# Kernel tuning notes

Measured on AMD Instinct MI355X. Metric: run time of the kernel, lower is better.

Reference implementation:

```python
import jax, jax.numpy as jnp
import numpy as np

B, L, D, V = 4096, 200, 64, 100000
ATTR_LEN = (2, 6, 10)  # label_size = 18
NEG = -1e9


def setup_inputs() -> dict:
    key = jax.random.key(0)
    ks = jax.random.split(key, 12)
    x = jax.random.randint(ks[0], (B, L), 0, V)
    lengths = jax.random.randint(ks[1], (B,), 1, L + 1)  # ragged valid lengths >= 1
    x_mask = jnp.arange(L)[None, :] < lengths[:, None]   # prefix-valid bool mask [B,L]
    y = (jax.random.uniform(ks[2], (B, sum(ATTR_LEN))) < 0.5).astype(jnp.float32)
    ob = (jax.random.uniform(ks[3], (B, sum(ATTR_LEN))) < 0.8).astype(jnp.float32)
    emb_table = (jax.random.normal(ks[4], (V, D)) * 0.02).at[0].set(0.0)  # padding_idx=0
    tran_W = jax.random.normal(ks[5], (3, D, D)) * 0.05   # emb_tran Linear weights (per attr)
    tran_b = jnp.zeros((3, D))
    att_W = jax.random.normal(ks[6], (3, D)) * 0.05       # item_att_W: Linear(D,1) per attr
    att_b = jnp.zeros((3,))
    W0 = jax.random.normal(ks[7], (D, ATTR_LEN[0])) * 0.05  # W_all (no bias)
    W1 = jax.random.normal(ks[8], (D, ATTR_LEN[1])) * 0.05
    W2 = jax.random.normal(ks[9], (D, ATTR_LEN[2])) * 0.05
    return {"x": x, "x_mask": x_mask, "y": y, "ob": ob, "emb_table": emb_table,
            "tran_W": tran_W, "tran_b": tran_b, "att_W": att_W, "att_b": att_b,
            "W0": W0, "W1": W1, "W2": W2}


def reference(x, x_mask, y, ob, emb_table, tran_W, tran_b, att_W, att_b, W0, W1, W2):
    # embed: [B,L,D]
    embed = emb_table[x]
    # per-attribute transformed embeddings: [3,B,L,D]
    e = jax.nn.relu(jnp.einsum('bld,ade->able', embed, tran_W) + tran_b[:, None, None, :])
    # attention logits per attribute: [3,B,L]
    att_u = jax.nn.relu(jnp.einsum('able,ae->abl', e, att_W) + att_b[:, None, None])
    # masked softmax over valid prefix (equivalent to the per-sample length loop)
    m = x_mask.astype(e.dtype)
    scores = jnp.where(x_mask[None, :, :], att_u, NEG)
    att = jax.nn.softmax(scores, axis=-1) * m[None, :, :]
    # attention-pooled user representation per attribute: [3,B,D]
    rep = jnp.tanh(jnp.einsum('abl,able->abe', att, e))
    # torch: cat([rep_a.unsqueeze(2)],2).view(B,-1) -> interleaved (d-major, attr-minor) layout
    user_flat = jnp.transpose(rep, (1, 2, 0)).reshape(rep.shape[1], -1)  # [B, 3*D]
    Ddim = emb_table.shape[1]
    W_user = jnp.concatenate([user_flat[:, 0 * Ddim:1 * Ddim] @ W0,
                              user_flat[:, 1 * Ddim:2 * Ddim] @ W1,
                              user_flat[:, 2 * Ddim:3 * Ddim] @ W2], axis=1)
    # W_compact = W_user * ob  (observed-label mask)
    return W_user * ob
```

## Files before the change

kernel.cpp:

```cpp
#include <hip/hip_runtime.h>

typedef unsigned int u32;
typedef unsigned short u16;
typedef unsigned char u8;
typedef unsigned long long u64;

typedef __attribute__((ext_vector_type(8))) short bf16x8;
typedef __attribute__((ext_vector_type(4))) float f32x4;
typedef __attribute__((ext_vector_type(4))) u32 u32x4;

#define L_SEQ 200

__device__ __forceinline__ u16 f2bf(float f) {
    u32 u = __float_as_uint(f);
    return (u16)((u + 0x7FFFu + ((u >> 16) & 1u)) >> 16);
}
__device__ __forceinline__ u32 pk2bf(float fx, float fy) {
    u32 xb = __float_as_uint(fx) + 0x8000u;
    u32 yb = __float_as_uint(fy) + 0x8000u;
    return __byte_perm(xb, yb, 0x7632);
}

__device__ __forceinline__ float row16_sum(float v) {
    int x;
    x = __builtin_amdgcn_update_dpp(0, __float_as_int(v), 0x128, 0xF, 0xF, true);
    v += __int_as_float(x);
    x = __builtin_amdgcn_update_dpp(0, __float_as_int(v), 0x124, 0xF, 0xF, true);
    v += __int_as_float(x);
    x = __builtin_amdgcn_update_dpp(0, __float_as_int(v), 0x122, 0xF, 0xF, true);
    v += __int_as_float(x);
    x = __builtin_amdgcn_update_dpp(0, __float_as_int(v), 0x121, 0xF, 0xF, true);
    v += __int_as_float(x);
    return v;
}
__device__ __forceinline__ float wave_sumf(float v) {
    v = row16_sum(v);
    v += __shfl_xor(v, 16, 64);
    v += __shfl_xor(v, 32, 64);
    return v;
}

__global__ __launch_bounds__(256) void etna_prep(const void* __restrict__ xmask,
                                                 const float* __restrict__ tranW,
                                                 const float* __restrict__ emb,
                                                 void* __restrict__ ws, int Bn, int Vn,
                                                 int doConv) {
    const int tid = threadIdx.x;
    const int bid = blockIdx.x;

    if (doConv) {
        u64* dst = (u64*)((char*)ws + 40960);
        const float4* src = (const float4*)emb;
        int ng = Vn * 16;
        for (int i = bid * 256 + tid; i < ng; i += gridDim.x * 256) {
            float4 v = src[i];
            u64 lo = pk2bf(v.x, v.y);
            u64 hi = pk2bf(v.z, v.w);
            dst[i] = lo | (hi << 32);
        }
    }

    if (bid < 48) {
        int it = bid * 256 + tid;
        int jj = it & 7;
        int ln = (it >> 3) & 63;
        int kh = (it >> 9) & 1;
        int c = (it >> 10) & 3;
        int a = it >> 12;
        int k = kh * 32 + (ln >> 4) * 8 + jj;
        int n = c * 16 + (ln & 15);
        ((u16*)ws)[it] = f2bf(tranW[a * 4096 + k * 64 + n]);
        return;
    }

    const int wv = tid >> 6;
    const int lane = tid & 63;
    int esz;
    {
        u32 accF = 0, acc0 = 0, accO = 0;
#pragma unroll
        for (int k = 0; k < 4; ++k) {
            int i = lane + 64 * k;
            u32 w = (i < 200) ? ((const u32*)xmask)[i] : 0u;
            accF |= (w & 0xFEFEFEFEu);
            acc0 |= (w & 0x000000FFu);
            accO |= (w & 0xFFFFFF00u);
        }
        bool isFloat = __ballot(accF != 0) != 0;
        bool hasB0   = __ballot(acc0 != 0) != 0;
        bool hasOdd  = __ballot(accO != 0) != 0;
        esz = isFloat ? (hasB0 ? 2 : 4) : (hasOdd ? 1 : 4);
    }
    int s = (bid - 48) * 4 + wv;
    if (s < Bn) {
        int len = 0;
        int mbase = s * L_SEQ;
#pragma unroll
        for (int c4 = 0; c4 < 4; ++c4) {
            int l = c4 * 64 + lane;
            bool v = false;
            if (l < L_SEQ) {
                int off = mbase + l;
                if (esz == 1)      v = ((const u8*)xmask)[off] != 0;
                else if (esz == 2) v = ((const u16*)xmask)[off] != 0;
                else               v = ((const u32*)xmask)[off] != 0;
            }
            len += (int)__popcll(__ballot(v));
        }
        if (lane == 0) ((int*)((char*)ws + 24576))[s] = len;
    }
}

template <bool TAB>
__global__ __launch_bounds__(384, 4) void etna_mfma(
    const int* __restrict__ x, const float* __restrict__ ob,
    const float* __restrict__ emb, const float* __restrict__ tranb,
    const float* __restrict__ attW, const float* __restrict__ attb,
    const float* __restrict__ W0, const float* __restrict__ W1,
    const float* __restrict__ W2, float* __restrict__ out,
    const void* __restrict__ ws, int Vn) {
    __shared__ float pN[2][3][64];
    __shared__ float pD[2][3];
    __shared__ float repl[3][64];

    const int tid = threadIdx.x;
    const int w = tid >> 6;
    const int a = w % 3;
    const int h = w / 3;
    const int lane = tid & 63;
    const int col = lane & 15;
    const int g = lane >> 4;
    const int b = blockIdx.x;

    const u16* wsBf = (const u16*)ws;
    bf16x8 Bf[4][2];
#pragma unroll
    for (int c = 0; c < 4; ++c)
#pragma unroll
        for (int kh = 0; kh < 2; ++kh)
            Bf[c][kh] = *(const bf16x8*)&wsBf[(((a * 4 + c) * 2 + kh) * 64 + lane) * 8];

    const int len = ((const int*)((const char*)ws + 24576))[b];
    const u16* wsEmb = (const u16*)((const char*)ws + 40960);

    const float LOG2E = 1.44269504088896f;
    float TB[4], AW[4];
#pragma unroll
    for (int c = 0; c < 4; ++c) {
        TB[c] = tranb[a * 64 + c * 16 + col];
        AW[c] = attW[a * 64 + c * 16 + col] * LOG2E;
    }
    const float AB = attb[a] * LOG2E;

    const int* xrow = x + b * L_SEQ;

    auto loadId = [&](int t) -> int {
        int p = t * 16 + col;
        int q = (p < L_SEQ) ? p : (L_SEQ - 1);
        int id = xrow[q];
        id = max(0, min(id, Vn - 1));
        return (p < len) ? id : 0;
    };

    auto loadRow = [&](int id, bf16x8& r0, bf16x8& r1) {
        if (TAB) {
            const bf16x8* rp = (const bf16x8*)(wsEmb + (size_t)id * 64);
            r0 = rp[g];
            r1 = rp[4 + g];
        } else {
            const float4* ep4 = (const float4*)(emb + (size_t)id * 64);
            float4 q0 = ep4[2 * g], q1 = ep4[2 * g + 1];
            float4 q2 = ep4[8 + 2 * g], q3 = ep4[9 + 2 * g];
            u32x4 w0, w1;
            w0.x = pk2bf(q0.x, q0.y); w0.y = pk2bf(q0.z, q0.w);
            w0.z = pk2bf(q1.x, q1.y); w0.w = pk2bf(q1.z, q1.w);
            w1.x = pk2bf(q2.x, q2.y); w1.y = pk2bf(q2.z, q2.w);
            w1.z = pk2bf(q3.x, q3.y); w1.w = pk2bf(q3.z, q3.w);
            r0 = __builtin_bit_cast(bf16x8, w0);
            r1 = __builtin_bit_cast(bf16x8, w1);
        }
    };

    const int nt = (len + 15) >> 4;
    const int nth = (nt + 1) >> 1;
    const int tA = h * nth;
    const int tB = min(nt, tA + nth);

    float NUM[4] = {0.f, 0.f, 0.f, 0.f};
    float DEN = 0.f;

    bf16x8 a0, a1;
    int idN = 0;
    if (tA < tB) {
        int id0 = loadId(tA);
        loadRow(id0, a0, a1);
        idN = loadId(tA + 1);
    }

    for (int t = tA; t < tB; ++t) {
        bf16x8 n0 = a0, n1 = a1;
        if (t + 1 < tB) loadRow(idN, n0, n1);
        idN = loadId(t + 2);

        f32x4 E[4];
#pragma unroll
        for (int c = 0; c < 4; ++c) {
            f32x4 cc = {TB[c], TB[c], TB[c], TB[c]};
            cc = __builtin_amdgcn_mfma_f32_16x16x32_bf16(a0, Bf[c][0], cc, 0, 0, 0);
            cc = __builtin_amdgcn_mfma_f32_16x16x32_bf16(a1, Bf[c][1], cc, 0, 0, 0);
            E[c].x = fmaxf(cc.x, 0.f);
            E[c].y = fmaxf(cc.y, 0.f);
            E[c].z = fmaxf(cc.z, 0.f);
            E[c].w = fmaxf(cc.w, 0.f);
        }
        float p0 = E[0].x * AW[0] + E[1].x * AW[1] + E[2].x * AW[2] + E[3].x * AW[3];
        float p1 = E[0].y * AW[0] + E[1].y * AW[1] + E[2].y * AW[2] + E[3].y * AW[3];
        float p2 = E[0].z * AW[0] + E[1].z * AW[1] + E[2].z * AW[2] + E[3].z * AW[3];
        float p3 = E[0].w * AW[0] + E[1].w * AW[1] + E[2].w * AW[2] + E[3].w * AW[3];
        p0 = row16_sum(p0);
        p1 = row16_sum(p1);
        p2 = row16_sum(p2);
        p3 = row16_sum(p3);

        int lrow = (t << 4) + 4 * g;
        float u0 = fmaxf(p0 + AB, 0.f);
        float u1 = fmaxf(p1 + AB, 0.f);
        float u2 = fmaxf(p2 + AB, 0.f);
        float u3 = fmaxf(p3 + AB, 0.f);
        float s0 = (lrow + 0 < len) ? exp2f(u0) : 0.f;
        float s1 = (lrow + 1 < len) ? exp2f(u1) : 0.f;
        float s2 = (lrow + 2 < len) ? exp2f(u2) : 0.f;
        float s3 = (lrow + 3 < len) ? exp2f(u3) : 0.f;
        DEN += s0 + s1 + s2 + s3;
#pragma unroll
        for (int c = 0; c < 4; ++c)
            NUM[c] += s0 * E[c].x + s1 * E[c].y + s2 * E[c].z + s3 * E[c].w;

        a0 = n0;
        a1 = n1;
    }

    {
        float d = DEN;
        d += __shfl_xor(d, 16, 64);
        d += __shfl_xor(d, 32, 64);
        if (lane == 0) pD[h][a] = d;
#pragma unroll
        for (int c = 0; c < 4; ++c) {
            float v = NUM[c];
            v += __shfl_xor(v, 16, 64);
            v += __shfl_xor(v, 32, 64);
            if (g == 0) pN[h][a][c * 16 + col] = v;
        }
    }
    __syncthreads();

    if (h == 0) {
        float dt = pD[0][a] + pD[1][a];
        float rden = 1.0f / fmaxf(dt, 1e-20f);
        float nv = pN[0][a][lane] + pN[1][a][lane];
        repl[a][lane] = tanhf(nv * rden);
    }
    __syncthreads();

    {
        const int AL = (a == 0) ? 2 : (a == 1 ? 6 : 10);
        const int OFF = (a == 0) ? 0 : (a == 1 ? 2 : 8);
        const float* Wp = (a == 0) ? W0 : (a == 1 ? W1 : W2);
        int gg = a * 64 + lane;
        float v = repl[gg % 3][gg / 3];
        for (int k = h; k < AL; k += 2) {
            float pz = wave_sumf(v * Wp[lane * AL + k]);
            if (lane == 0) out[b * 18 + OFF + k] = pz * ob[b * 18 + OFF + k];
        }
    }
}

extern "C" void kernel_launch(void* const* d_in, const int* in_sizes, int n_in,
                              void* d_out, int out_size, void* d_ws, size_t ws_size,
                              hipStream_t stream) {
    const int* x = (const int*)d_in[0];
    const void* xmask = d_in[1];
    const float* ob = (const float*)d_in[3];
    const float* emb = (const float*)d_in[4];
    const float* tranW = (const float*)d_in[5];
    const float* tranb = (const float*)d_in[6];
    const float* attW = (const float*)d_in[7];
    const float* attb = (const float*)d_in[8];
    const float* W0 = (const float*)d_in[9];
    const float* W1 = (const float*)d_in[10];
    const float* W2 = (const float*)d_in[11];

    const int Bn = in_sizes[0] / L_SEQ;
    const int Vn = in_sizes[4] / 64;

    const size_t need = 40960 + (size_t)Vn * 128;
    const int useTab = (ws_size >= need) ? 1 : 0;

    etna_prep<<<48 + (Bn + 3) / 4, 256, 0, stream>>>(xmask, tranW, emb, d_ws, Bn, Vn, useTab);
    if (useTab)
        etna_mfma<true><<<Bn, 384, 0, stream>>>(x, ob, emb, tranb, attW, attb,
                                                W0, W1, W2, (float*)d_out, d_ws, Vn);
    else
        etna_mfma<false><<<Bn, 384, 0, stream>>>(x, ob, emb, tranb, attW, attb,
                                                 W0, W1, W2, (float*)d_out, d_ws, Vn);
}
```

Before: 168.9 us.

## Stage gathered embedding rows in swizzled LDS shared by all three attribute waves

Previously each of six waves (3 attributes x 2 halves of the sequence) gathered the same embedding rows from global memory on its own, so every row was fetched three times. Now the block uses three waves, one per attribute. They cooperatively gather each sample's valid rows once into an XOR-swizzled LDS tile through a short register pipeline, then each wave runs its MFMA loop over the whole sequence reading from LDS. This cuts redundant global gathers and removes the cross-half partial reduction. In exchange it adds about 26KB of LDS per block, which may limit occupancy, halves the wave-level parallelism per sample, and puts a serial staging phase before compute.

Result: faster. 148.0 us (-12.4%).

```diff
diff --git a/kernel.cpp b/kernel.cpp
--- a/kernel.cpp
+++ b/kernel.cpp
@@ -10,6 +10,8 @@
 typedef __attribute__((ext_vector_type(4))) u32 u32x4;
 
 #define L_SEQ 200
+#define ST_ROWS 208
+#define RND_MAX 9
 
 __device__ __forceinline__ u16 f2bf(float f) {
     u32 u = __float_as_uint(f);
@@ -112,21 +114,18 @@
 }
 
 template <bool TAB>
-__global__ __launch_bounds__(384, 4) void etna_mfma(
+__global__ __launch_bounds__(192, 4) void etna_mfma(
     const int* __restrict__ x, const float* __restrict__ ob,
     const float* __restrict__ emb, const float* __restrict__ tranb,
     const float* __restrict__ attW, const float* __restrict__ attb,
     const float* __restrict__ W0, const float* __restrict__ W1,
     const float* __restrict__ W2, float* __restrict__ out,
     const void* __restrict__ ws, int Vn) {
-    __shared__ float pN[2][3][64];
-    __shared__ float pD[2][3];
-    __shared__ float repl[3][64];
+    __shared__ __align__(16) float ldsf[ST_ROWS * 32];
+    char* ldsb = (char*)ldsf;
 
     const int tid = threadIdx.x;
-    const int w = tid >> 6;
-    const int a = w % 3;
-    const int h = w / 3;
+    const int a = tid >> 6;
     const int lane = tid & 63;
     const int col = lane & 15;
     const int g = lane >> 4;
@@ -153,54 +152,76 @@
     const float AB = attb[a] * LOG2E;
 
     const int* xrow = x + b * L_SEQ;
-
-    auto loadId = [&](int t) -> int {
-        int p = t * 16 + col;
-        int q = (p < L_SEQ) ? p : (L_SEQ - 1);
-        int id = xrow[q];
-        id = max(0, min(id, Vn - 1));
-        return (p < len) ? id : 0;
-    };
-
-    auto loadRow = [&](int id, bf16x8& r0, bf16x8& r1) {
-        if (TAB) {
-            const bf16x8* rp = (const bf16x8*)(wsEmb + (size_t)id * 64);
-            r0 = rp[g];
-            r1 = rp[4 + g];
-        } else {
-            const float4* ep4 = (const float4*)(emb + (size_t)id * 64);
-            float4 q0 = ep4[2 * g], q1 = ep4[2 * g + 1];
-            float4 q2 = ep4[8 + 2 * g], q3 = ep4[9 + 2 * g];
-            u32x4 w0, w1;
-            w0.x = pk2bf(q0.x, q0.y); w0.y = pk2bf(q0.z, q0.w);
-            w0.z = pk2bf(q1.x, q1.y); w0.w = pk2bf(q1.z, q1.w);
-            w1.x = pk2bf(q2.x, q2.y); w1.y = pk2bf(q2.z, q2.w);
-            w1.z = pk2bf(q3.x, q3.y); w1.w = pk2bf(q3.z, q3.w);
-            r0 = __builtin_bit_cast(bf16x8, w0);
-            r1 = __builtin_bit_cast(bf16x8, w1);
-        }
-    };
-
     const int nt = (len + 15) >> 4;
-    const int nth = (nt + 1) >> 1;
-    const int tA = h * nth;
-    const int tB = min(nt, tA + nth);
+    const int stRows = nt << 4;
+    const int rounds = (stRows + 23) / 24;
+
+    const int sp = a * 8 + (lane >> 3);
+    const int ch = lane & 7;
+
+    int ids[RND_MAX];
+#pragma unroll
+    for (int j = 0; j < RND_MAX; ++j) {
+        ids[j] = 0;
+        if (j < rounds) {
+            int p = j * 24 + sp;
+            int q = (p < L_SEQ) ? p : (L_SEQ - 1);
+            int idv = xrow[q];
+            idv = max(0, min(idv, Vn - 1));
+            ids[j] = (p < len) ? idv : 0;
+        }
+    }
+
+    if (TAB) {
+        bf16x8 stq[3];
+#pragma unroll
+        for (int j = 0; j < RND_MAX + 2; ++j) {
+            if (j < RND_MAX && j < rounds)
+                stq[j % 3] = ((const bf16x8*)(wsEmb + (size_t)ids[j] * 64))[ch];
+            int k = j - 2;
+            if (k >= 0 && k < rounds) {
+                int p = k * 24 + sp;
+                if (p < stRows) {
+                    u32 off = (u32)p * 128 + (u32)((ch * 16) ^ ((p & 7) << 4));
+                    *(bf16x8*)(ldsb + off) = stq[k % 3];
+                }
+            }
+        }
+    } else {
+        for (int j = 0; j < rounds; ++j) {
+            int p = j * 24 + sp;
+            if (p < stRows) {
+                const float4* ep4 = (const float4*)(emb + (size_t)ids[j] * 64);
+                float4 q0 = ep4[2 * ch], q1 = ep4[2 * ch + 1];
+                u32x4 wv_;
+                wv_.x = pk2bf(q0.x, q0.y);
+                wv_.y = pk2bf(q0.z, q0.w);
+                wv_.z = pk2bf(q1.x, q1.y);
+                wv_.w = pk2bf(q1.z, q1.w);
+                u32 off = (u32)p * 128 + (u32)((ch * 16) ^ ((p & 7) << 4));
+                *(bf16x8*)(ldsb + off) = __builtin_bit_cast(bf16x8, wv_);
+            }
+        }
+    }
+    __syncthreads();
+
+    const u32 c0 = (u32)((g * 16) ^ ((col & 7) << 4));
+    u32 ra = (u32)col * 128 + c0;
 
     float NUM[4] = {0.f, 0.f, 0.f, 0.f};
     float DEN = 0.f;
 
-    bf16x8 a0, a1;
-    int idN = 0;
-    if (tA < tB) {
-        int id0 = loadId(tA);
-        loadRow(id0, a0, a1);
-        idN = loadId(tA + 1);
-    }
-
-    for (int t = tA; t < tB; ++t) {
+    bf16x8 a0 = *(const bf16x8*)(ldsb + ra);
+    bf16x8 a1 = *(const bf16x8*)(ldsb + (ra ^ 64u));
+
+    for (int t = 0; t < nt; ++t) {
         bf16x8 n0 = a0, n1 = a1;
-        if (t + 1 < tB) loadRow(idN, n0, n1);
-        idN = loadId(t + 2);
+        if (t + 1 < nt) {
+            u32 rn = ra + 2048u;
+            n0 = *(const bf16x8*)(ldsb + rn);
+            n1 = *(const bf16x8*)(ldsb + (rn ^ 64u));
+        }
+        ra += 2048u;
 
         f32x4 E[4];
 #pragma unroll
@@ -240,26 +261,20 @@
         a1 = n1;
     }
 
+    __syncthreads();
+
     {
         float d = DEN;
         d += __shfl_xor(d, 16, 64);
         d += __shfl_xor(d, 32, 64);
-        if (lane == 0) pD[h][a] = d;
+        float rden = 1.0f / fmaxf(d, 1e-20f);
 #pragma unroll
         for (int c = 0; c < 4; ++c) {
             float v = NUM[c];
             v += __shfl_xor(v, 16, 64);
             v += __shfl_xor(v, 32, 64);
-            if (g == 0) pN[h][a][c * 16 + col] = v;
-        }
-    }
-    __syncthreads();
-
-    if (h == 0) {
-        float dt = pD[0][a] + pD[1][a];
-        float rden = 1.0f / fmaxf(dt, 1e-20f);
-        float nv = pN[0][a][lane] + pN[1][a][lane];
-        repl[a][lane] = tanhf(nv * rden);
+            if (g == 0) ldsf[a * 64 + c * 16 + col] = tanhf(v * rden);
+        }
     }
     __syncthreads();
 
@@ -268,8 +283,8 @@
         const int OFF = (a == 0) ? 0 : (a == 1 ? 2 : 8);
         const float* Wp = (a == 0) ? W0 : (a == 1 ? W1 : W2);
         int gg = a * 64 + lane;
-        float v = repl[gg % 3][gg / 3];
-        for (int k = h; k < AL; k += 2) {
+        float v = ldsf[(gg % 3) * 64 + gg / 3];
+        for (int k = 0; k < AL; ++k) {
             float pz = wave_sumf(v * Wp[lane * AL + k]);
             if (lane == 0) out[b * 18 + OFF + k] = pz * ob[b * 18 + OFF + k];
         }
@@ -299,9 +314,9 @@
 
     etna_prep<<<48 + (Bn + 3) / 4, 256, 0, stream>>>(xmask, tranW, emb, d_ws, Bn, Vn, useTab);
     if (useTab)
-        etna_mfma<true><<<Bn, 384, 0, stream>>>(x, ob, emb, tranb, attW, attb,
+        etna_mfma<true><<<Bn, 192, 0, stream>>>(x, ob, emb, tranb, attW, attb,
                                                 W0, W1, W2, (float*)d_out, d_ws, Vn);
     else
-        etna_mfma<false><<<Bn, 384, 0, stream>>>(x, ob, emb, tranb, attW, attb,
+        etna_mfma<false><<<Bn, 192, 0, stream>>>(x, ob, emb, tranb, attW, attb,
                                                  W0, W1, W2, (float*)d_out, d_ws, Vn);
 }
```
